# Optimization experiments

Hardware: AMD Instinct MI355X
Metric: run time of the kernel (lower is better)

The kernel has to match this reference:

```python
import jax, jax.numpy as jnp
import numpy as np

B, F, C, T, K, P = 16, 32, 32, 2048, 129, 64  # P = conv padding; K-1-P = 64 -> same-length output


def setup_inputs() -> dict:
    key = jax.random.key(0)
    k0, k1, k2, k3, k4, k5 = jax.random.split(key, 6)
    coeffs = jax.random.normal(k0, (B, 2, F, 7, 5, T), dtype=jnp.float32)
    rows = jax.random.randint(k1, (C,), 0, 7, dtype=jnp.int32)
    cols = jax.random.randint(k2, (C,), 0, 5, dtype=jnp.int32)
    ri_scale = jax.random.uniform(k3, (F,), jnp.float32, 0.5, 1.5)
    ri_shift = jax.random.normal(k4, (F,), dtype=jnp.float32) * 0.1
    freq_gain = jnp.ones((F,), dtype=jnp.float32)
    # torch ConvTranspose1d weight: (in_channels=C*2F, out_channels/groups=1, K)
    synth_weight = jax.random.normal(k5, (C * 2 * F, 1, K), dtype=jnp.float32) / np.sqrt(2.0 * F * K)
    return {"coeffs": coeffs, "rows": rows, "cols": cols, "ri_scale": ri_scale,
            "ri_shift": ri_shift, "freq_gain": freq_gain, "synth_weight": synth_weight}


def reference(coeffs, rows, cols, ri_scale, ri_shift, freq_gain, synth_weight):
    Bc, _, Fq, _, _, Tt = coeffs.shape
    Cc = rows.shape[0]
    # fancy-index gather over the (7,5) electrode grid -> (B, 2, F, C, T)
    feat = coeffs[:, :, :, rows, cols, :]
    # normalize (ri stats broadcast over freq dim) then per-frequency gain
    fdim = (None, None, slice(None), None, None)
    feat = feat / (ri_scale[fdim] + 1e-12) - ri_shift[fdim]
    feat = feat * freq_gain[fdim]
    # permute (B,2,F,C,T) -> (B,C,2,F,T) and flatten to (B, C*2F, T)
    z = jnp.transpose(feat, (0, 3, 1, 2, 4)).reshape(Bc, Cc * 2 * Fq, Tt)
    # depthwise-grouped ConvTranspose1d (stride=1, padding=P) == grouped
    # cross-correlation with time-flipped kernel and padding K-1-P.
    Kk = synth_weight.shape[-1]
    w = synth_weight.reshape(Cc, 2 * Fq, Kk)[:, :, ::-1]  # (Cout=C, Cin/groups=2F, K)
    pad = Kk - 1 - P
    x_hat = jax.lax.conv_general_dilated(
        z, w, window_strides=(1,), padding=[(pad, pad)],
        feature_group_count=Cc, dimension_numbers=("NCH", "OIH", "NCH"))
    return x_hat  # (B, C, T)
```

## Files before the change

### kernel.cpp

```cpp
#include <hip/hip_runtime.h>

typedef __attribute__((ext_vector_type(8))) short short8;
typedef __attribute__((ext_vector_type(4))) float f32x4;

#define C_ 32
#define T_ 2048
#define K_ 129
#define ZROWS (12 * 8 * 16)
#define ZS_USHORT (ZROWS * 24)

__device__ __forceinline__ unsigned int bfround(float f) {
    unsigned int u = __float_as_uint(f);
    return u + 0x7fffu + ((u >> 16) & 1u);
}

__global__ __launch_bounds__(256) void wtoep_pack(
    const float* __restrict__ sw, unsigned short* __restrict__ wt)
{
    const int c = blockIdx.x, dd = blockIdx.y;
    const int t = threadIdx.x, l = t & 63, fw = t >> 6;
    const int m = l & 15, qb = (l >> 4) & 1, i2 = (l >> 5) & 1;
    const int d = dd - 4;
    for (int fr = fw; fr < 32; fr += 4) {
        const int iq = fr >> 2, igl = fr & 3;
        const int i = iq * 8 + igl * 2 + i2;
        unsigned short v[8];
        #pragma unroll
        for (int e = 0; e < 8; ++e) {
            const int tl = 8 * qb + e;
            const int j = 16 * d + 64 + m - tl;
            const float wv = (j >= 0 && j <= 128) ? sw[(c * 64 + i) * K_ + j] : 0.f;
            v[e] = (unsigned short)(bfround(wv) >> 16);
        }
        *(short8*)(wt + (((c * 9 + dd) * 32 + fr) * 64 + l) * 8) = *(short8*)v;
    }
}

__global__ __launch_bounds__(256, 2) void wavelet_synth_v4(
    const float* __restrict__ coeffs, const int* __restrict__ rows,
    const int* __restrict__ cols, const float* __restrict__ ri_scale,
    const float* __restrict__ ri_shift, const float* __restrict__ freq_gain,
    const unsigned short* __restrict__ wt, float* __restrict__ out)
{
    __shared__ __align__(16) unsigned short zs[ZS_USHORT];

    const int t  = threadIdx.x;
    const int g0 = blockIdx.x * 4;
    const int c  = blockIdx.y;
    const int rc = rows[c];
    const int cc = cols[c];

    const int lane = t & 63;
    const int w    = t >> 6;
    const int i2   = (lane >> 5) & 1;
    const int qb   = (lane >> 4) & 1;

    f32x4 acc0 = {0,0,0,0}, acc1 = {0,0,0,0}, acc2 = {0,0,0,0}, acc3 = {0,0,0,0};

    const int s_r  = t & 1;
    const int s_b  = (t >> 1) & 15;
    const int s_il = (t >> 5) & 7;

    for (int iq = 0; iq < 8; ++iq) {
        __syncthreads();
        for (int p = 0; p < 12; ++p) {
            const int cn = p * 256 + t;
            const int vi = cn >> 8;
            const int il = s_il + ((p & 1) ? 0 : 0);
            const int ilf = (cn >> 5) & 7;
            const int v_abs = g0 - 4 + vi;
            const int i  = iq * 8 + ilf;
            const int f  = i & 31;
            const int ri = i >> 5;
            float vv[8];
            if (v_abs >= 0 && v_abs < 128) {
                const float inv = __builtin_amdgcn_rcpf(ri_scale[f] + 1e-12f);
                const float Aa  = inv * freq_gain[f];
                const float Bb  = -ri_shift[f] * freq_gain[f];
                const long  row = ((long)(s_b * 2 + ri) * 32 + f) * 35 + rc * 5 + cc;
                const float* src = coeffs + row * T_ + v_abs * 16 + s_r * 8;
                const float4 x = *(const float4*)(src);
                const float4 y = *(const float4*)(src + 4);
                vv[0] = x.x * Aa + Bb; vv[1] = x.y * Aa + Bb;
                vv[2] = x.z * Aa + Bb; vv[3] = x.w * Aa + Bb;
                vv[4] = y.x * Aa + Bb; vv[5] = y.y * Aa + Bb;
                vv[6] = y.z * Aa + Bb; vv[7] = y.w * Aa + Bb;
            } else {
                #pragma unroll
                for (int e = 0; e < 8; ++e) vv[e] = 0.f;
            }
            unsigned short pk[8];
            #pragma unroll
            for (int e = 0; e < 8; ++e) pk[e] = (unsigned short)(bfround(vv[e]) >> 16);
            *(short8*)(zs + ((vi * 8 + ilf) * 16 + s_b) * 24 + s_r * 8) = *(short8*)pk;
        }
        __syncthreads();

        const unsigned short* wbase = wt + ((c * 9) * 32 + iq * 4 + w) * 512 + lane * 8;
        for (int d = 0; d < 9; ++d) {
            const short8 afrag = *(const short8*)(wbase + d * 32 * 512);
            const int vbase = 8 - d;
            const unsigned short* zb =
                zs + ((w * 2 + i2) * 16 + (lane & 15)) * 24 + qb * 8;
            const short8 b0 = *(const short8*)(zb + (vbase + 0) * (8 * 16 * 24));
            acc0 = __builtin_amdgcn_mfma_f32_16x16x32_bf16(afrag, b0, acc0, 0, 0, 0);
            const short8 b1 = *(const short8*)(zb + (vbase + 1) * (8 * 16 * 24));
            acc1 = __builtin_amdgcn_mfma_f32_16x16x32_bf16(afrag, b1, acc1, 0, 0, 0);
            const short8 b2 = *(const short8*)(zb + (vbase + 2) * (8 * 16 * 24));
            acc2 = __builtin_amdgcn_mfma_f32_16x16x32_bf16(afrag, b2, acc2, 0, 0, 0);
            const short8 b3 = *(const short8*)(zb + (vbase + 3) * (8 * 16 * 24));
            acc3 = __builtin_amdgcn_mfma_f32_16x16x32_bf16(afrag, b3, acc3, 0, 0, 0);
        }
    }

    __syncthreads();
    float* red = (float*)zs;
    *(f32x4*)(red + ((w * 4 + 0) * 64 + lane) * 4) = acc0;
    *(f32x4*)(red + ((w * 4 + 1) * 64 + lane) * 4) = acc1;
    *(f32x4*)(red + ((w * 4 + 2) * 64 + lane) * 4) = acc2;
    *(f32x4*)(red + ((w * 4 + 3) * 64 + lane) * 4) = acc3;
    __syncthreads();

    {
        const int s  = t & 3;
        const int b  = (t >> 2) & 15;
        const int g  = t >> 6;
        float4 o;
        float* po = (float*)&o;
        #pragma unroll
        for (int rr = 0; rr < 4; ++rr) {
            float sum = 0.f;
            #pragma unroll
            for (int ww = 0; ww < 4; ++ww)
                sum += red[((ww * 4 + g) * 64 + s * 16 + b) * 4 + rr];
            po[rr] = sum;
        }
        *(float4*)(out + ((long)b * C_ + c) * T_ + (g0 + g) * 16 + s * 4) = o;
    }
}

extern "C" void kernel_launch(void* const* d_in, const int* in_sizes, int n_in,
                              void* d_out, int out_size, void* d_ws, size_t ws_size,
                              hipStream_t stream) {
    const float* coeffs    = (const float*)d_in[0];
    const int*   rows      = (const int*)d_in[1];
    const int*   cols      = (const int*)d_in[2];
    const float* ri_scale  = (const float*)d_in[3];
    const float* ri_shift  = (const float*)d_in[4];
    const float* freq_gain = (const float*)d_in[5];
    const float* sw        = (const float*)d_in[6];
    float* out = (float*)d_out;
    unsigned short* wt = (unsigned short*)d_ws;

    hipLaunchKernelGGL(wtoep_pack, dim3(32, 9), dim3(256), 0, stream, sw, wt);
    hipLaunchKernelGGL(wavelet_synth_v4, dim3(32, 32), dim3(256), 0, stream,
                       coeffs, rows, cols, ri_scale, ri_shift, freq_gain, wt, out);
}
```

Measured before the change: 457.4 us.

## Move conv halo from input loads to output atomic scatter

Each block now loads and normalizes only its own 4 time-blocks of coefficients, instead of 12 blocks including the input halo. The Toeplitz MFMA results go into 12 output-shifted accumulators, and the halo is pushed to neighbouring output blocks with float atomic adds into a zeroed output. This removes the threefold redundant global gather and bf16 conversion per block. The smaller LDS footprint allows three blocks per CU. In exchange it adds a memset, three times as many output writes done as atomics, and a non-deterministic summation order.

```diff
diff --git a/kernel.cpp b/kernel.cpp
--- a/kernel.cpp
+++ b/kernel.cpp
@@ -6,8 +6,6 @@
 #define C_ 32
 #define T_ 2048
 #define K_ 129
-#define ZROWS (12 * 8 * 16)
-#define ZS_USHORT (ZROWS * 24)
 
 __device__ __forceinline__ unsigned int bfround(float f) {
     unsigned int u = __float_as_uint(f);
@@ -36,13 +34,14 @@
     }
 }
 
-__global__ __launch_bounds__(256, 2) void wavelet_synth_v4(
+__global__ __launch_bounds__(256, 3) void wavelet_synth_v5(
     const float* __restrict__ coeffs, const int* __restrict__ rows,
     const int* __restrict__ cols, const float* __restrict__ ri_scale,
     const float* __restrict__ ri_shift, const float* __restrict__ freq_gain,
     const unsigned short* __restrict__ wt, float* __restrict__ out)
 {
-    __shared__ __align__(16) unsigned short zs[ZS_USHORT];
+    __shared__ __align__(16) unsigned char smem[49152];
+    unsigned short* zs = (unsigned short*)smem;
 
     const int t  = threadIdx.x;
     const int g0 = blockIdx.x * 4;
@@ -55,87 +54,79 @@
     const int i2   = (lane >> 5) & 1;
     const int qb   = (lane >> 4) & 1;
 
-    f32x4 acc0 = {0,0,0,0}, acc1 = {0,0,0,0}, acc2 = {0,0,0,0}, acc3 = {0,0,0,0};
-
     const int s_r  = t & 1;
     const int s_b  = (t >> 1) & 15;
     const int s_il = (t >> 5) & 7;
 
+    f32x4 acc[12];
+    #pragma unroll
+    for (int a = 0; a < 12; ++a) acc[a] = (f32x4){0.f, 0.f, 0.f, 0.f};
+
     for (int iq = 0; iq < 8; ++iq) {
+        const int i  = iq * 8 + s_il;
+        const int f  = i & 31;
+        const int ri = i >> 5;
+        const float inv = __builtin_amdgcn_rcpf(ri_scale[f] + 1e-12f);
+        const float Aa  = inv * freq_gain[f];
+        const float Bb  = -ri_shift[f] * freq_gain[f];
+        const long  row = ((long)(s_b * 2 + ri) * 32 + f) * 35 + rc * 5 + cc;
+        const float* srcb = coeffs + row * T_ + g0 * 16 + s_r * 8;
+
         __syncthreads();
-        for (int p = 0; p < 12; ++p) {
-            const int cn = p * 256 + t;
-            const int vi = cn >> 8;
-            const int il = s_il + ((p & 1) ? 0 : 0);
-            const int ilf = (cn >> 5) & 7;
-            const int v_abs = g0 - 4 + vi;
-            const int i  = iq * 8 + ilf;
-            const int f  = i & 31;
-            const int ri = i >> 5;
+        #pragma unroll
+        for (int vi = 0; vi < 4; ++vi) {
+            const float4 x = *(const float4*)(srcb + vi * 16);
+            const float4 y = *(const float4*)(srcb + vi * 16 + 4);
             float vv[8];
-            if (v_abs >= 0 && v_abs < 128) {
-                const float inv = __builtin_amdgcn_rcpf(ri_scale[f] + 1e-12f);
-                const float Aa  = inv * freq_gain[f];
-                const float Bb  = -ri_shift[f] * freq_gain[f];
-                const long  row = ((long)(s_b * 2 + ri) * 32 + f) * 35 + rc * 5 + cc;
-                const float* src = coeffs + row * T_ + v_abs * 16 + s_r * 8;
-                const float4 x = *(const float4*)(src);
-                const float4 y = *(const float4*)(src + 4);
-                vv[0] = x.x * Aa + Bb; vv[1] = x.y * Aa + Bb;
-                vv[2] = x.z * Aa + Bb; vv[3] = x.w * Aa + Bb;
-                vv[4] = y.x * Aa + Bb; vv[5] = y.y * Aa + Bb;
-                vv[6] = y.z * Aa + Bb; vv[7] = y.w * Aa + Bb;
-            } else {
-                #pragma unroll
-                for (int e = 0; e < 8; ++e) vv[e] = 0.f;
-            }
+            vv[0] = x.x * Aa + Bb; vv[1] = x.y * Aa + Bb;
+            vv[2] = x.z * Aa + Bb; vv[3] = x.w * Aa + Bb;
+            vv[4] = y.x * Aa + Bb; vv[5] = y.y * Aa + Bb;
+            vv[6] = y.z * Aa + Bb; vv[7] = y.w * Aa + Bb;
             unsigned short pk[8];
             #pragma unroll
             for (int e = 0; e < 8; ++e) pk[e] = (unsigned short)(bfround(vv[e]) >> 16);
-            *(short8*)(zs + ((vi * 8 + ilf) * 16 + s_b) * 24 + s_r * 8) = *(short8*)pk;
+            *(short8*)(zs + ((vi * 8 + s_il) * 16 + s_b) * 24 + s_r * 8) = *(short8*)pk;
         }
         __syncthreads();
 
         const unsigned short* wbase = wt + ((c * 9) * 32 + iq * 4 + w) * 512 + lane * 8;
+        const unsigned short* zb =
+            zs + ((w * 2 + i2) * 16 + (lane & 15)) * 24 + qb * 8;
+        #pragma unroll
         for (int d = 0; d < 9; ++d) {
             const short8 afrag = *(const short8*)(wbase + d * 32 * 512);
-            const int vbase = 8 - d;
-            const unsigned short* zb =
-                zs + ((w * 2 + i2) * 16 + (lane & 15)) * 24 + qb * 8;
-            const short8 b0 = *(const short8*)(zb + (vbase + 0) * (8 * 16 * 24));
-            acc0 = __builtin_amdgcn_mfma_f32_16x16x32_bf16(afrag, b0, acc0, 0, 0, 0);
-            const short8 b1 = *(const short8*)(zb + (vbase + 1) * (8 * 16 * 24));
-            acc1 = __builtin_amdgcn_mfma_f32_16x16x32_bf16(afrag, b1, acc1, 0, 0, 0);
-            const short8 b2 = *(const short8*)(zb + (vbase + 2) * (8 * 16 * 24));
-            acc2 = __builtin_amdgcn_mfma_f32_16x16x32_bf16(afrag, b2, acc2, 0, 0, 0);
-            const short8 b3 = *(const short8*)(zb + (vbase + 3) * (8 * 16 * 24));
-            acc3 = __builtin_amdgcn_mfma_f32_16x16x32_bf16(afrag, b3, acc3, 0, 0, 0);
+            #pragma unroll
+            for (int vi = 0; vi < 4; ++vi) {
+                const short8 bf = *(const short8*)(zb + vi * (8 * 16 * 24));
+                acc[vi + d] = __builtin_amdgcn_mfma_f32_16x16x32_bf16(
+                    afrag, bf, acc[vi + d], 0, 0, 0);
+            }
         }
     }
 
     __syncthreads();
-    float* red = (float*)zs;
-    *(f32x4*)(red + ((w * 4 + 0) * 64 + lane) * 4) = acc0;
-    *(f32x4*)(red + ((w * 4 + 1) * 64 + lane) * 4) = acc1;
-    *(f32x4*)(red + ((w * 4 + 2) * 64 + lane) * 4) = acc2;
-    *(f32x4*)(red + ((w * 4 + 3) * 64 + lane) * 4) = acc3;
+    float* red = (float*)smem;
+    #pragma unroll
+    for (int a = 0; a < 12; ++a)
+        *(f32x4*)(red + ((w * 12 + a) * 64 + lane) * 4) = acc[a];
     __syncthreads();
 
     {
-        const int s  = t & 3;
-        const int b  = (t >> 2) & 15;
-        const int g  = t >> 6;
-        float4 o;
-        float* po = (float*)&o;
+        const int rb  = t >> 4;
+        const int tau = t & 15;
+        const int s   = tau >> 2;
+        const int rr  = tau & 3;
+        float* obase = out + ((long)rb * C_ + c) * T_ + tau;
         #pragma unroll
-        for (int rr = 0; rr < 4; ++rr) {
+        for (int a = 0; a < 12; ++a) {
+            const int o = g0 - 4 + a;
+            if (o < 0 || o >= 128) continue;
             float sum = 0.f;
             #pragma unroll
             for (int ww = 0; ww < 4; ++ww)
-                sum += red[((ww * 4 + g) * 64 + s * 16 + b) * 4 + rr];
-            po[rr] = sum;
+                sum += red[((ww * 12 + a) * 64 + s * 16 + rb) * 4 + rr];
+            unsafeAtomicAdd(obase + o * 16, sum);
         }
-        *(float4*)(out + ((long)b * C_ + c) * T_ + (g0 + g) * 16 + s * 4) = o;
     }
 }
 
@@ -152,7 +143,8 @@
     float* out = (float*)d_out;
     unsigned short* wt = (unsigned short*)d_ws;
 
+    hipMemsetAsync(d_out, 0, (size_t)out_size, stream);
     hipLaunchKernelGGL(wtoep_pack, dim3(32, 9), dim3(256), 0, stream, sw, wt);
-    hipLaunchKernelGGL(wavelet_synth_v4, dim3(32, 32), dim3(256), 0, stream,
+    hipLaunchKernelGGL(wavelet_synth_v5, dim3(32, 32), dim3(256), 0, stream,
                        coeffs, rows, cols, ri_scale, ri_shift, freq_gain, wt, out);
 }
```

After: 412.5 us. 1.11x faster.
